# Kernel optimization log

Hardware: AMD Instinct MI355X
Metric: run time of the kernel (lower is better)

Reference implementation:

```python
import jax, jax.numpy as jnp
import numpy as np
import math

# ---- module hyperparameters (match init_kwargs) ----
B = 2            # batch
CTX = 512        # context_length
C = 16           # n_subspaces
RS = 16          # rank_subspace
RT = 16          # rank_transformations
T = 2 + 2 * RT   # 34 transformation slots
L = int(math.isqrt(CTX * C * 2))  # latent_dim = 128
K = int(math.isqrt(L))            # 11
H, W = 1024, 1024                 # output_shape
EPS = 1e-12


def siglog(x):
    # dyna.functional.siglog: sign(x) * log(1 + |x|)
    return jnp.sign(x) * jnp.log1p(jnp.abs(x))


def linear_interp_last(x, out_size):
    """F.interpolate(mode='linear', align_corners=False) along last axis."""
    in_size = x.shape[-1]
    scale = in_size / out_size
    pos = (jnp.arange(out_size, dtype=jnp.float32) + 0.5) * scale - 0.5
    pos = jnp.clip(pos, 0.0, in_size - 1)
    i0 = jnp.floor(pos).astype(jnp.int32)
    i1 = jnp.minimum(i0 + 1, in_size - 1)
    w = (pos - i0.astype(jnp.float32)).astype(x.dtype)
    return x[..., i0] * (1.0 - w) + x[..., i1] * w


def setup_inputs() -> dict:
    key = jax.random.key(0)
    ks = jax.random.split(key, 8)
    x = jax.random.normal(ks[0], (B, CTX), dtype=jnp.float32)
    # nn.Linear(CTX, L*4): store weight as [in, out]
    W_ctx = jax.random.normal(ks[1], (CTX, L * 4), dtype=jnp.float32) / np.sqrt(CTX)
    b_ctx = jax.random.normal(ks[2], (L * 4,), dtype=jnp.float32) * 0.01
    space_i = jax.random.normal(ks[3], (1, C, RS, H, 2), dtype=jnp.float32)
    space_j = jax.random.normal(ks[4], (1, C, RS, W, 2), dtype=jnp.float32)
    # xavier-ish scale for the CP factors
    gA = np.sqrt(2.0 / (L + K))
    A = jax.random.normal(ks[5], (T, C, L, K, RS, 2), dtype=jnp.float32) * gA
    Bf = jax.random.normal(ks[6], (T, C, K, L, RS, 2), dtype=jnp.float32) * gA
    return {"x": x, "W_ctx": W_ctx, "b_ctx": b_ctx, "A": A, "Bf": Bf,
            "space_i": space_i, "space_j": space_j}


def _apply_space(space, shift, z, size):
    # space: [1,C,RS,size,2]; shift: [B,C,RS,2]; z: [B,RT,C,RS,2]
    sp = space + shift[:, :, :, None, :]                     # [B,C,RS,size,2]
    z = jnp.transpose(z, (0, 4, 2, 3, 1))                    # [B,2,C,RS,RT]
    z = linear_interp_last(z, size)                          # [B,2,C,RS,size]
    z = jnp.transpose(z, (0, 2, 3, 4, 1))                    # [B,C,RS,size,2]
    prod = sp * z
    re = prod[..., 1:] - prod[..., :1]                       # diff over last dim (size 2)
    im = (sp * z[..., ::-1]).sum(axis=-1, keepdims=True)     # a0*z1 + a1*z0
    return jnp.concatenate([re, im], axis=-1)                # [B,C,RS,size,2]


def reference(x, W_ctx, b_ctx, A, Bf, space_i, space_j):
    # context transform + siglog modulation
    xt = x @ W_ctx + b_ctx                                   # [B, 4L]
    s = 2 * L
    xm = (xt[:, :s] * siglog(xt[:, s:])).reshape(-1, L, 2)   # [B,L,2]
    xr, xi = xm[..., 0], xm[..., 1]                          # [B,L]

    # Complex broadcast einsums: i = x * A (btclki), j = x * B (btclkj).
    # (i*j).sum(k) == x^2 * sum_k(A[t,c,l,k,r] * B[t,c,k,l,r])  (complex)
    Ar, Ai = A[..., 0], A[..., 1]                            # [T,C,L,K,RS]
    Br, Bi = Bf[..., 0], Bf[..., 1]                          # [T,C,K,L,RS]
    ABr = jnp.einsum('tclkr,tcklr->tclr', Ar, Br) - jnp.einsum('tclkr,tcklr->tclr', Ai, Bi)
    ABi = jnp.einsum('tclkr,tcklr->tclr', Ar, Bi) + jnp.einsum('tclkr,tcklr->tclr', Ai, Br)
    x2r = xr * xr - xi * xi                                  # [B,L]
    x2i = 2.0 * xr * xi
    x2r_b = x2r[:, None, None, :, None]                      # [B,1,1,L,1]
    x2i_b = x2i[:, None, None, :, None]
    Re = x2r_b * ABr[None] - x2i_b * ABi[None]               # [B,T,C,L,RS]
    Im = x2r_b * ABi[None] + x2i_b * ABr[None]

    # polar normalization + magnitude-weighted averaging over L (dim 3)
    mag = jnp.sqrt(Re * Re + Im * Im + EPS)
    cos_t = Re / mag
    sin_t = Im / mag
    msum = mag.sum(axis=3)
    cosw = (cos_t * mag).sum(axis=3) / (msum + EPS)          # [B,T,C,RS]
    sinw = (sin_t * mag).sum(axis=3) / (msum + EPS)
    mag_mean = mag.mean(axis=3)
    tr = jnp.stack([cosw * mag_mean, sinw * mag_mean], axis=-1)  # [B,T,C,RS,2]

    out_i = _apply_space(space_i, tr[:, 0], tr[:, 2:2 + RT], H)
    out_j = _apply_space(space_j, tr[:, 1], tr[:, 2 + RT:2 + 2 * RT], W)
    return out_i, out_j
```

## Files before the change

### kernel.cpp

```cpp
#include <hip/hip_runtime.h>
#include <math.h>

#define B_   2
#define CTX_ 512
#define C_   16
#define RS_  16
#define RT_  16
#define T_   34
#define L_   128
#define K_   11
#define H_   1024
#define EPS_ 1e-12f

#define NSPLIT_ 4
#define LCHUNK_ 32

__device__ __forceinline__ float siglog(float v) {
    return copysignf(log1pf(fabsf(v)), v);
}

__global__ __launch_bounds__(512) void k_ctx(const float* __restrict__ x,
                                             const float* __restrict__ Wc,
                                             const float* __restrict__ bc,
                                             float2* __restrict__ x2out) {
    __shared__ float xrow[CTX_];
    __shared__ float xt[4 * L_];
    const int b = blockIdx.x;
    const int tid = threadIdx.x;
    xrow[tid] = x[b * CTX_ + tid];
    __syncthreads();
    float sum = bc[tid];
#pragma unroll 8
    for (int c = 0; c < CTX_; ++c)
        sum = fmaf(xrow[c], Wc[c * (4 * L_) + tid], sum);
    xt[tid] = sum;
    __syncthreads();
    if (tid < L_) {
        float xr = xt[2 * tid]     * siglog(xt[2 * L_ + 2 * tid]);
        float xi = xt[2 * tid + 1] * siglog(xt[2 * L_ + 2 * tid + 1]);
        x2out[b * L_ + tid] = make_float2(xr * xr - xi * xi, 2.0f * xr * xi);
    }
}

__global__ __launch_bounds__(256, 4) void k_tr_part(const float4* __restrict__ A4,
                                                    const float4* __restrict__ B4,
                                                    const float2* __restrict__ x2,
                                                    float* __restrict__ part) {
    const int blk = blockIdx.x;
    const int tc  = blk / NSPLIT_;
    const int s   = blk % NSPLIT_;
    const int tid = threadIdx.x;
    const int rp  = tid & 7;
    const int l   = s * LCHUNK_ + (tid >> 3);

    const float4* __restrict__ Ab = A4 + ((size_t)(tc * L_ + l) * K_) * 8 + rp;
    const float4* __restrict__ Bb = B4 + ((size_t)tc * K_ * L_ + l) * 8 + rp;

    float4 a[K_];
    float4 bv[K_];
#pragma unroll
    for (int k = 0; k < K_; ++k) a[k]  = Ab[(size_t)k * 8];
#pragma unroll
    for (int k = 0; k < K_; ++k) bv[k] = Bb[(size_t)k * L_ * 8];

    float2 xv0 = x2[0 * L_ + l];
    float2 xv1 = x2[1 * L_ + l];

    float abr0 = 0.f, abi0 = 0.f, abr1 = 0.f, abi1 = 0.f;
#pragma unroll
    for (int k = 0; k < K_; ++k) {
        abr0 = fmaf(a[k].x, bv[k].x, abr0); abr0 = fmaf(-a[k].y, bv[k].y, abr0);
        abi0 = fmaf(a[k].x, bv[k].y, abi0); abi0 = fmaf( a[k].y, bv[k].x, abi0);
        abr1 = fmaf(a[k].z, bv[k].z, abr1); abr1 = fmaf(-a[k].w, bv[k].w, abr1);
        abi1 = fmaf(a[k].z, bv[k].w, abi1); abi1 = fmaf( a[k].w, bv[k].z, abi1);
    }

    float acc[12];
    {
        float Re0 = xv0.x * abr0 - xv0.y * abi0;
        float Im0 = xv0.x * abi0 + xv0.y * abr0;
        float Re1 = xv0.x * abr1 - xv0.y * abi1;
        float Im1 = xv0.x * abi1 + xv0.y * abr1;
        acc[0] = Re0; acc[1] = Im0;
        acc[2] = sqrtf(fmaf(Re0, Re0, fmaf(Im0, Im0, EPS_)));
        acc[3] = Re1; acc[4] = Im1;
        acc[5] = sqrtf(fmaf(Re1, Re1, fmaf(Im1, Im1, EPS_)));
    }
    {
        float Re0 = xv1.x * abr0 - xv1.y * abi0;
        float Im0 = xv1.x * abi0 + xv1.y * abr0;
        float Re1 = xv1.x * abr1 - xv1.y * abi1;
        float Im1 = xv1.x * abi1 + xv1.y * abr1;
        acc[6] = Re0; acc[7] = Im0;
        acc[8] = sqrtf(fmaf(Re0, Re0, fmaf(Im0, Im0, EPS_)));
        acc[9] = Re1; acc[10] = Im1;
        acc[11] = sqrtf(fmaf(Re1, Re1, fmaf(Im1, Im1, EPS_)));
    }

#pragma unroll
    for (int off = 8; off <= 32; off <<= 1) {
#pragma unroll
        for (int i = 0; i < 12; ++i)
            acc[i] += __shfl_xor(acc[i], off);
    }

    __shared__ float wred[4][8][12];
    const int wave = tid >> 6;
    const int lane = tid & 63;
    if (lane < 8) {
#pragma unroll
        for (int i = 0; i < 12; ++i) wred[wave][lane][i] = acc[i];
    }
    __syncthreads();

    if (tid < 96) {
        const int rpi  = tid / 12;
        const int comp = tid % 12;
        float v = wred[0][rpi][comp] + wred[1][rpi][comp]
                + wred[2][rpi][comp] + wred[3][rpi][comp];
        const int b    = comp / 6;
        const int pair = (comp / 3) & 1;
        const int c3   = comp % 3;
        const int r    = 2 * rpi + pair;
        part[(((size_t)blk * B_ + b) * RS_ + r) * 3 + c3] = v;
    }
}

__global__ __launch_bounds__(256) void k_tr_fin(const float* __restrict__ part,
                                                float2* __restrict__ tr2) {
    const int idx = blockIdx.x * blockDim.x + threadIdx.x;
    const int total = T_ * C_ * B_ * RS_;
    if (idx >= total) return;
    const int r  = idx & 15;
    const int b  = (idx >> 4) & 1;
    const int tc = idx >> 5;

    float a0 = 0.f, a1 = 0.f, a2 = 0.f;
#pragma unroll
    for (int s = 0; s < NSPLIT_; ++s) {
        const size_t base = (((size_t)(tc * NSPLIT_ + s) * B_ + b) * RS_ + r) * 3;
        a0 += part[base + 0];
        a1 += part[base + 1];
        a2 += part[base + 2];
    }
    const float inv = a2 / ((a2 + EPS_) * (float)L_);
    const int t = tc / C_, c = tc % C_;
    tr2[(((size_t)b * T_ + t) * C_ + c) * RS_ + r] = make_float2(a0 * inv, a1 * inv);
}

__global__ __launch_bounds__(256) void k_out(const float2* __restrict__ space_i,
                                             const float2* __restrict__ space_j,
                                             const float2* __restrict__ tr2,
                                             float2* __restrict__ out) {
    const int half = B_ * C_ * RS_ * H_;
    int idx = blockIdx.x * blockDim.x + threadIdx.x;
    if (idx >= 2 * half) return;
    const int which = (idx >= half) ? 1 : 0;
    int id = idx - which * half;

    const int h = id & (H_ - 1);
    int rest = id >> 10;
    const int r = rest & 15; rest >>= 4;
    const int c = rest & 15;
    const int b = rest >> 4;

    const float2* __restrict__ sp2 = which ? space_j : space_i;

    const size_t trb = (((size_t)b * T_) * C_ + c) * RS_ + r;
    const size_t trs = (size_t)C_ * RS_;

    const float2 sh = tr2[trb + (size_t)which * trs];

    float pos = (h + 0.5f) * (16.0f / 1024.0f) - 0.5f;
    pos = fminf(fmaxf(pos, 0.0f), 15.0f);
    const int i0 = (int)floorf(pos);
    const int i1 = min(i0 + 1, RT_ - 1);
    const float w = pos - (float)i0;

    const int tb = 2 + which * RT_;
    const float2 z0 = tr2[trb + (size_t)(tb + i0) * trs];
    const float2 z1 = tr2[trb + (size_t)(tb + i1) * trs];
    const float zx = z0.x * (1.0f - w) + z1.x * w;
    const float zy = z0.y * (1.0f - w) + z1.y * w;

    const float2 sv = sp2[((size_t)c * RS_ + r) * H_ + h];
    const float sx = sv.x + sh.x;
    const float sy = sv.y + sh.y;

    out[idx] = make_float2(sy * zy - sx * zx, sx * zy + sy * zx);
}

extern "C" void kernel_launch(void* const* d_in, const int* in_sizes, int n_in,
                              void* d_out, int out_size, void* d_ws, size_t ws_size,
                              hipStream_t stream) {
    const float*  x  = (const float*)d_in[0];
    const float*  Wc = (const float*)d_in[1];
    const float*  bc = (const float*)d_in[2];
    const float4* A4 = (const float4*)d_in[3];
    const float4* B4 = (const float4*)d_in[4];
    const float2* si = (const float2*)d_in[5];
    const float2* sj = (const float2*)d_in[6];

    float2* x2   = (float2*)d_ws;
    float*  part = (float*)((char*)d_ws + 4096);
    float2* tr2  = (float2*)((char*)d_ws + 4096 + 1024 * 1024);

    k_ctx<<<B_, 512, 0, stream>>>(x, Wc, bc, x2);

    k_tr_part<<<T_ * C_ * NSPLIT_, 256, 0, stream>>>(A4, B4, x2, part);

    const int fin_total = T_ * C_ * B_ * RS_;
    k_tr_fin<<<(fin_total + 255) / 256, 256, 0, stream>>>(part, tr2);

    const int total = 2 * B_ * C_ * RS_ * H_;
    k_out<<<(total + 255) / 256, 256, 0, stream>>>(si, sj, tr2, (float2*)d_out);
}
```

Measured before the change: 66.28 us.

## Fuse split-L finalize into output kernel via atomics and vectorize output stores

Removes the k_tr_fin kernel. The partial reductions are now accumulated with atomicAdd into a zeroed buffer (a hipMemsetAsync is added), and the output kernel computes the normalized transform values inline from the accumulated sums. The output kernel now processes two h positions per thread with float4 loads and nontemporal float4 stores. It also changes the unroll and launch-bounds settings and adds a sched_barrier. The trade is one kernel launch and intermediate buffer removed, in exchange for a memset, atomic contention and redundant per-thread finalize arithmetic.

```diff
diff --git a/kernel.cpp b/kernel.cpp
--- a/kernel.cpp
+++ b/kernel.cpp
@@ -12,8 +12,11 @@
 #define H_   1024
 #define EPS_ 1e-12f
 
-#define NSPLIT_ 4
-#define LCHUNK_ 32
+#define NSPLIT_  4
+#define LCHUNK_  32
+#define NBLKTR_  (T_ * C_ * NSPLIT_)
+
+typedef float vfloat4 __attribute__((ext_vector_type(4)));
 
 __device__ __forceinline__ float siglog(float v) {
     return copysignf(log1pf(fabsf(v)), v);
@@ -30,7 +33,7 @@
     xrow[tid] = x[b * CTX_ + tid];
     __syncthreads();
     float sum = bc[tid];
-#pragma unroll 8
+#pragma unroll 16
     for (int c = 0; c < CTX_; ++c)
         sum = fmaf(xrow[c], Wc[c * (4 * L_) + tid], sum);
     xt[tid] = sum;
@@ -42,13 +45,13 @@
     }
 }
 
-__global__ __launch_bounds__(256, 4) void k_tr_part(const float4* __restrict__ A4,
+__global__ __launch_bounds__(256, 2) void k_tr_part(const float4* __restrict__ A4,
                                                     const float4* __restrict__ B4,
-                                                    const float2* __restrict__ x2,
+                                                    const float2* __restrict__ x2g,
                                                     float* __restrict__ part) {
     const int blk = blockIdx.x;
-    const int tc  = blk / NSPLIT_;
-    const int s   = blk % NSPLIT_;
+    const int tc  = blk >> 2;
+    const int s   = blk & 3;
     const int tid = threadIdx.x;
     const int rp  = tid & 7;
     const int l   = s * LCHUNK_ + (tid >> 3);
@@ -62,9 +65,10 @@
     for (int k = 0; k < K_; ++k) a[k]  = Ab[(size_t)k * 8];
 #pragma unroll
     for (int k = 0; k < K_; ++k) bv[k] = Bb[(size_t)k * L_ * 8];
-
-    float2 xv0 = x2[0 * L_ + l];
-    float2 xv1 = x2[1 * L_ + l];
+    const float2 xv0 = x2g[l];
+    const float2 xv1 = x2g[L_ + l];
+
+    __builtin_amdgcn_sched_barrier(0);
 
     float abr0 = 0.f, abi0 = 0.f, abr1 = 0.f, abi1 = 0.f;
 #pragma unroll
@@ -122,72 +126,68 @@
         const int pair = (comp / 3) & 1;
         const int c3   = comp % 3;
         const int r    = 2 * rpi + pair;
-        part[(((size_t)blk * B_ + b) * RS_ + r) * 3 + c3] = v;
-    }
-}
-
-__global__ __launch_bounds__(256) void k_tr_fin(const float* __restrict__ part,
-                                                float2* __restrict__ tr2) {
-    const int idx = blockIdx.x * blockDim.x + threadIdx.x;
-    const int total = T_ * C_ * B_ * RS_;
-    if (idx >= total) return;
-    const int r  = idx & 15;
-    const int b  = (idx >> 4) & 1;
-    const int tc = idx >> 5;
-
-    float a0 = 0.f, a1 = 0.f, a2 = 0.f;
-#pragma unroll
-    for (int s = 0; s < NSPLIT_; ++s) {
-        const size_t base = (((size_t)(tc * NSPLIT_ + s) * B_ + b) * RS_ + r) * 3;
-        a0 += part[base + 0];
-        a1 += part[base + 1];
-        a2 += part[base + 2];
-    }
+        atomicAdd(&part[(((size_t)tc * B_ + b) * RS_ + r) * 3 + c3], v);
+    }
+}
+
+__device__ __forceinline__ float2 tr_at(const float* __restrict__ part,
+                                        int t, int c, int b, int r) {
+    const int tc = t * C_ + c;
+    const size_t base = (((size_t)tc * B_ + b) * RS_ + r) * 3;
+    const float a0 = part[base + 0];
+    const float a1 = part[base + 1];
+    const float a2 = part[base + 2];
     const float inv = a2 / ((a2 + EPS_) * (float)L_);
-    const int t = tc / C_, c = tc % C_;
-    tr2[(((size_t)b * T_ + t) * C_ + c) * RS_ + r] = make_float2(a0 * inv, a1 * inv);
-}
-
-__global__ __launch_bounds__(256) void k_out(const float2* __restrict__ space_i,
-                                             const float2* __restrict__ space_j,
-                                             const float2* __restrict__ tr2,
-                                             float2* __restrict__ out) {
-    const int half = B_ * C_ * RS_ * H_;
+    return make_float2(a0 * inv, a1 * inv);
+}
+
+__global__ __launch_bounds__(256) void k_out(const float4* __restrict__ space_i4,
+                                             const float4* __restrict__ space_j4,
+                                             const float* __restrict__ part,
+                                             float4* __restrict__ out4) {
+    const int halfq = B_ * C_ * RS_ * H_ / 2;
     int idx = blockIdx.x * blockDim.x + threadIdx.x;
-    if (idx >= 2 * half) return;
-    const int which = (idx >= half) ? 1 : 0;
-    int id = idx - which * half;
-
-    const int h = id & (H_ - 1);
-    int rest = id >> 10;
+    if (idx >= 2 * halfq) return;
+    const int which = (idx >= halfq) ? 1 : 0;
+    int id = idx - which * halfq;
+
+    const int h2 = id & (H_ / 2 - 1);
+    int rest = id >> 9;
     const int r = rest & 15; rest >>= 4;
     const int c = rest & 15;
     const int b = rest >> 4;
 
-    const float2* __restrict__ sp2 = which ? space_j : space_i;
-
-    const size_t trb = (((size_t)b * T_) * C_ + c) * RS_ + r;
-    const size_t trs = (size_t)C_ * RS_;
-
-    const float2 sh = tr2[trb + (size_t)which * trs];
-
-    float pos = (h + 0.5f) * (16.0f / 1024.0f) - 0.5f;
-    pos = fminf(fmaxf(pos, 0.0f), 15.0f);
-    const int i0 = (int)floorf(pos);
-    const int i1 = min(i0 + 1, RT_ - 1);
-    const float w = pos - (float)i0;
-
+    const float4* __restrict__ sp4 = which ? space_j4 : space_i4;
+
+    const float2 sh = tr_at(part, which, c, b, r);
     const int tb = 2 + which * RT_;
-    const float2 z0 = tr2[trb + (size_t)(tb + i0) * trs];
-    const float2 z1 = tr2[trb + (size_t)(tb + i1) * trs];
-    const float zx = z0.x * (1.0f - w) + z1.x * w;
-    const float zy = z0.y * (1.0f - w) + z1.y * w;
-
-    const float2 sv = sp2[((size_t)c * RS_ + r) * H_ + h];
-    const float sx = sv.x + sh.x;
-    const float sy = sv.y + sh.y;
-
-    out[idx] = make_float2(sy * zy - sx * zx, sx * zy + sy * zx);
+
+    const float4 sv = sp4[((size_t)c * RS_ + r) * (H_ / 2) + h2];
+
+    float res[4];
+#pragma unroll
+    for (int u = 0; u < 2; ++u) {
+        const int h = 2 * h2 + u;
+        float pos = (h + 0.5f) * (16.0f / 1024.0f) - 0.5f;
+        pos = fminf(fmaxf(pos, 0.0f), 15.0f);
+        const int i0 = (int)floorf(pos);
+        const int i1 = min(i0 + 1, RT_ - 1);
+        const float w = pos - (float)i0;
+
+        const float2 z0 = tr_at(part, tb + i0, c, b, r);
+        const float2 z1 = tr_at(part, tb + i1, c, b, r);
+        const float zx = z0.x * (1.0f - w) + z1.x * w;
+        const float zy = z0.y * (1.0f - w) + z1.y * w;
+
+        const float sx = (u ? sv.z : sv.x) + sh.x;
+        const float sy = (u ? sv.w : sv.y) + sh.y;
+
+        res[2 * u + 0] = sy * zy - sx * zx;
+        res[2 * u + 1] = sx * zy + sy * zx;
+    }
+    vfloat4 rv;
+    rv.x = res[0]; rv.y = res[1]; rv.z = res[2]; rv.w = res[3];
+    __builtin_nontemporal_store(rv, (vfloat4*)&out4[idx]);
 }
 
 extern "C" void kernel_launch(void* const* d_in, const int* in_sizes, int n_in,
@@ -198,20 +198,19 @@
     const float*  bc = (const float*)d_in[2];
     const float4* A4 = (const float4*)d_in[3];
     const float4* B4 = (const float4*)d_in[4];
-    const float2* si = (const float2*)d_in[5];
-    const float2* sj = (const float2*)d_in[6];
+    const float4* si = (const float4*)d_in[5];
+    const float4* sj = (const float4*)d_in[6];
 
     float2* x2   = (float2*)d_ws;
     float*  part = (float*)((char*)d_ws + 4096);
-    float2* tr2  = (float2*)((char*)d_ws + 4096 + 1024 * 1024);
+
+    const size_t part_bytes = (size_t)T_ * C_ * B_ * RS_ * 3 * sizeof(float);
+    (void)hipMemsetAsync(part, 0, part_bytes, stream);
 
     k_ctx<<<B_, 512, 0, stream>>>(x, Wc, bc, x2);
 
-    k_tr_part<<<T_ * C_ * NSPLIT_, 256, 0, stream>>>(A4, B4, x2, part);
-
-    const int fin_total = T_ * C_ * B_ * RS_;
-    k_tr_fin<<<(fin_total + 255) / 256, 256, 0, stream>>>(part, tr2);
-
-    const int total = 2 * B_ * C_ * RS_ * H_;
-    k_out<<<(total + 255) / 256, 256, 0, stream>>>(si, sj, tr2, (float2*)d_out);
-}
+    k_tr_part<<<NBLKTR_, 256, 0, stream>>>(A4, B4, x2, part);
+
+    const int totalq = 2 * B_ * C_ * RS_ * H_ / 2;
+    k_out<<<(totalq + 255) / 256, 256, 0, stream>>>(si, sj, part, (float4*)d_out);
+}
```

New measurement: 59.06 us. 10.9% less time.
